# Kernel tuning notes

Measured on AMD Instinct MI355X. Metric: run time of the kernel, lower is better.

Reference implementation:

```python
import jax, jax.numpy as jnp
import numpy as np

A = 5            # atten_size
WIN = 2 * A + 1  # window size = 11


def _xavier(key, shape):
    fan_in, fan_out = shape[-2], shape[-1]
    std = np.sqrt(2.0 / (fan_in + fan_out))
    return (jax.random.normal(key, shape, jnp.float32) * std).astype(jnp.float32)


def setup_inputs() -> dict:
    key = jax.random.key(0)
    ks = jax.random.split(key, 8)
    B, S, D, H, O = 32768, 11, 128, 32, 2
    return {
        "x": jax.random.normal(ks[0], (B, S, D), jnp.float32),
        "W1": _xavier(ks[1], (D, H)),
        "b1": jnp.zeros((1, 1, H), jnp.float32),
        "Wq": _xavier(ks[2], (H, H)),
        "Wk": _xavier(ks[3], (H, H)),
        "Wv": _xavier(ks[4], (H, H)),
        "pos_enc": _xavier(ks[5], (1, WIN, H)),
        "Wo": _xavier(ks[6], (H, O)),
        "bo": jnp.zeros((1, 1, O), jnp.float32),
    }


def reference(x, W1, b1, Wq, Wk, Wv, pos_enc, Wo, bo):
    B, S, D = x.shape
    H = W1.shape[1]
    h = jax.nn.relu(x @ W1 + b1)                 # (B,S,H)
    h = h + pos_enc[:, :S, :]
    # sliding-window neighborhood, equivalent to torch pad+roll+stack:
    # x_nei[b,t,i] = h[b, t + (A - i)] with zero padding out of range
    padded = jnp.pad(h, ((0, 0), (A, A), (0, 0)))
    x_nei = jnp.stack([padded[:, 2 * A - i: 2 * A - i + S, :] for i in range(WIN)], axis=2)
    q = (h @ Wq)[:, :, None, :]                  # (B,S,1,H)
    keys = x_nei @ Wk
    vals = x_nei @ Wv
    scores = jnp.matmul(q, jnp.swapaxes(keys, -1, -2)) / jnp.sqrt(jnp.float32(H))
    # Faithful to torch.nn.Softmax(2): softmax over the singleton dim -> all ones
    attn_w = jax.nn.softmax(scores, axis=2)
    attn_out = jnp.matmul(attn_w, vals)[:, :, 0, :]  # (B,S,H)
    out = attn_out @ Wo + bo                     # (B,S,O)
    return out, attn_w
```

## Files before the change

kernel.cpp:

```cpp
#include <hip/hip_runtime.h>
#include <stdint.h>

#define NB   32768
#define SS   11
#define DD   128
#define HH   32
#define ROWS (NB * SS)
#define RPB  128
#define NBLK (ROWS / RPB)
#define TPB  256
#define XSTRD 68
#define TOT4 (ROWS * SS / 4)
#define AUXOFF (ROWS * 2)

__device__ __forceinline__ uint32_t f2bf_u(float f) {
    uint32_t u = __float_as_uint(f);
    return (u + 0x7fffu + ((u >> 16) & 1u)) >> 16;
}
__device__ __forceinline__ uint32_t pkbf(float lo, float hi) {
    return f2bf_u(lo) | (f2bf_u(hi) << 16);
}
__device__ __forceinline__ float dot2bf(uint32_t a, uint32_t b, float c) {
    float d;
    asm("v_dot2_f32_bf16 %0, %1, %2, %3" : "=v"(d) : "v"(a), "v"(b), "v"(c));
    return d;
}
__device__ __forceinline__ float xor32sum(float v) {
    float a = v, b = v;
    asm("v_permlane32_swap_b32 %0, %1" : "+v"(a), "+v"(b));
    return a + b;
}

__global__ __launch_bounds__(64) void setup_kernel(
    const float* __restrict__ Wv, const float* __restrict__ Wo,
    const float* __restrict__ pos, const float* __restrict__ bo,
    float* __restrict__ aux)
{
    __shared__ float M_s[HH * 2];
    __shared__ float pm_s[SS * 2];
    const int t = threadIdx.x;
    {
        int j = t >> 1, o = t & 1;
        float s = 0.f;
        #pragma unroll 8
        for (int k = 0; k < HH; ++k) s += Wv[j * HH + k] * Wo[k * 2 + o];
        M_s[t] = s;
        aux[t] = s;
    }
    __syncthreads();
    if (t < 2 * SS) {
        int u = t >> 1, o = t & 1;
        float s = 0.f;
        #pragma unroll 8
        for (int j = 0; j < HH; ++j) s += pos[u * HH + j] * M_s[j * 2 + o];
        pm_s[t] = s;
    }
    __syncthreads();
    if (t < 2 * SS) {
        int tt = t >> 1, o = t & 1;
        int lo = tt - 5 < 0 ? 0 : tt - 5;
        int hi = tt + 5 > SS - 1 ? SS - 1 : tt + 5;
        float s = bo[o];
        for (int u = lo; u <= hi; ++u) s += pm_s[u * 2 + o];
        aux[64 + t] = s;
    }
}

__global__ __launch_bounds__(TPB, 3) void g_kernel(
    const float* __restrict__ x, const float* __restrict__ W1,
    const float* __restrict__ b1, const float* __restrict__ aux,
    float* __restrict__ g)
{
    __shared__ uint32_t x_p[RPB * XSTRD];
    __shared__ uint32_t w_p[64 * HH];

    const int t   = threadIdx.x;
    const int blk = blockIdx.x;

    const float4* xsrc = (const float4*)(x + (size_t)blk * (RPB * DD));
    #pragma unroll
    for (int k = 0; k < 8; ++k) {
        int j = t + k * TPB;
        float4 v0 = xsrc[2 * j], v1 = xsrc[2 * j + 1];
        uint4 pv;
        pv.x = pkbf(v0.x, v0.y); pv.y = pkbf(v0.z, v0.w);
        pv.z = pkbf(v1.x, v1.y); pv.w = pkbf(v1.z, v1.w);
        int row = j >> 4, d8 = j & 15;
        *(uint4*)&x_p[row * XSTRD + d8 * 4] = pv;
    }
    #pragma unroll
    for (int k = 0; k < 8; ++k) {
        int i = t + k * TPB;
        int p = i >> 5, j = i & 31;
        w_p[i] = pkbf(W1[(2 * p) * HH + j], W1[(2 * p + 1) * HH + j]);
    }

    const int lane = t & 63, wave = t >> 6;
    const int cg = lane & 3;
    const int rg = (lane >> 2) & 7;
    const int kc = lane >> 5;
    const int j0 = cg * 8;
    const int rbase = wave * 32 + rg;

    float b1v[8], Mv[16];
    *(float4*)&b1v[0] = *(const float4*)&b1[j0];
    *(float4*)&b1v[4] = *(const float4*)&b1[j0 + 4];
    #pragma unroll
    for (int q = 0; q < 4; ++q)
        *(float4*)&Mv[q * 4] = *(const float4*)&aux[j0 * 2 + q * 4];
    __syncthreads();

    float acc[4][8] = {};
    #pragma unroll
    for (int i = 0; i < 8; ++i) {
        uint32_t xv[4][4], wv[4][8];
        #pragma unroll
        for (int rr = 0; rr < 4; ++rr)
            *(uint4*)xv[rr] = *(const uint4*)&x_p[(rbase + 8 * rr) * XSTRD + kc * 32 + i * 4];
        #pragma unroll
        for (int pp = 0; pp < 4; ++pp) {
            *(uint4*)&wv[pp][0] = *(const uint4*)&w_p[(kc * 32 + i * 4 + pp) * HH + j0];
            *(uint4*)&wv[pp][4] = *(const uint4*)&w_p[(kc * 32 + i * 4 + pp) * HH + j0 + 4];
        }
        #pragma unroll
        for (int rr = 0; rr < 4; ++rr)
            #pragma unroll
            for (int pp = 0; pp < 4; ++pp)
                #pragma unroll
                for (int c = 0; c < 8; ++c)
                    acc[rr][c] = dot2bf(xv[rr][pp], wv[pp][c], acc[rr][c]);
    }

    #pragma unroll
    for (int rr = 0; rr < 4; ++rr) {
        float s0 = 0.f, s1 = 0.f;
        #pragma unroll
        for (int c = 0; c < 8; ++c) {
            float full = xor32sum(acc[rr][c]);
            float y = fmaxf(full + b1v[c], 0.f);
            s0 = fmaf(y, Mv[c * 2], s0);
            s1 = fmaf(y, Mv[c * 2 + 1], s1);
        }
        s0 += __shfl_xor(s0, 1); s1 += __shfl_xor(s1, 1);
        s0 += __shfl_xor(s0, 2); s1 += __shfl_xor(s1, 2);
        if ((lane & 35) == 0) {
            int row = blk * RPB + rbase + 8 * rr;
            ((float2*)g)[row] = make_float2(s0, s1);
        }
    }
}

__global__ __launch_bounds__(256) void outones_kernel(
    const float* __restrict__ g, const float* __restrict__ aux,
    float* __restrict__ out1, float4* __restrict__ attn)
{
    int idx = blockIdx.x * 256 + threadIdx.x;
    attn[idx] = make_float4(1.f, 1.f, 1.f, 1.f);
    if (idx < ROWS) {
        int b = idx / SS, tt = idx - b * SS;
        const float2* gb = (const float2*)(g + (size_t)b * (2 * SS));
        int lo = tt - 5 < 0 ? 0 : tt - 5;
        int hi = tt + 5 > SS - 1 ? SS - 1 : tt + 5;
        float2 pw = *(const float2*)&aux[64 + tt * 2];
        float s0 = pw.x, s1 = pw.y;
        for (int u = lo; u <= hi; ++u) { float2 v = gb[u]; s0 += v.x; s1 += v.y; }
        ((float2*)out1)[idx] = make_float2(s0, s1);
    }
}

__global__ __launch_bounds__(256) void out_kernel(
    const float* __restrict__ g, const float* __restrict__ aux,
    float* __restrict__ out1)
{
    int idx = blockIdx.x * 256 + threadIdx.x;
    int b = idx / SS, tt = idx - b * SS;
    const float2* gb = (const float2*)(g + (size_t)b * (2 * SS));
    int lo = tt - 5 < 0 ? 0 : tt - 5;
    int hi = tt + 5 > SS - 1 ? SS - 1 : tt + 5;
    float2 pw = *(const float2*)&aux[64 + tt * 2];
    float s0 = pw.x, s1 = pw.y;
    for (int u = lo; u <= hi; ++u) { float2 v = gb[u]; s0 += v.x; s1 += v.y; }
    ((float2*)out1)[idx] = make_float2(s0, s1);
}
__global__ __launch_bounds__(256) void ones_kernel(float4* __restrict__ p)
{
    int i = blockIdx.x * 256 + threadIdx.x;
    p[i] = make_float4(1.f, 1.f, 1.f, 1.f);
}

extern "C" void kernel_launch(void* const* d_in, const int* in_sizes, int n_in,
                              void* d_out, int out_size, void* d_ws, size_t ws_size,
                              hipStream_t stream)
{
    const float* x   = (const float*)d_in[0];
    const float* W1  = (const float*)d_in[1];
    const float* b1  = (const float*)d_in[2];
    const float* Wv  = (const float*)d_in[5];
    const float* pos = (const float*)d_in[6];
    const float* Wo  = (const float*)d_in[7];
    const float* bo  = (const float*)d_in[8];

    float* out1 = (float*)d_out;
    float* attn = out1 + (size_t)ROWS * 2;

    const bool ws_ok = ws_size >= (size_t)(AUXOFF + 128) * sizeof(float);
    float* base = ws_ok ? (float*)d_ws : attn;
    float* g    = base;
    float* aux  = base + AUXOFF;

    setup_kernel<<<1, 64, 0, stream>>>(Wv, Wo, pos, bo, aux);
    g_kernel<<<NBLK, TPB, 0, stream>>>(x, W1, b1, aux, g);
    if (ws_ok) {
        outones_kernel<<<TOT4 / 256, 256, 0, stream>>>(g, aux, out1, (float4*)attn);
    } else {
        out_kernel<<<ROWS / 256, 256, 0, stream>>>(g, aux, out1);
        ones_kernel<<<TOT4 / 256, 256, 0, stream>>>((float4*)attn);
    }
}
```

Baseline: 54.97 us.

## Make g_kernel persistent with register-prefetch of next x tile

Converts the main GEMM kernel into a persistent grid of 768 blocks that loop over tiles. While computing the current tile from LDS, each block loads the next tile's x into 16 float4 registers, then converts and stores it to LDS after a barrier. This overlaps global memory latency with compute and amortizes the W1 packing, at the cost of higher register pressure (the kernel still requests 3 blocks per SM) and extra barriers.

```diff
diff --git a/kernel.cpp b/kernel.cpp
--- a/kernel.cpp
+++ b/kernel.cpp
@@ -1,16 +1,17 @@
 #include <hip/hip_runtime.h>
 #include <stdint.h>
 
-#define NB   32768
-#define SS   11
-#define DD   128
-#define HH   32
-#define ROWS (NB * SS)
-#define RPB  128
-#define NBLK (ROWS / RPB)
-#define TPB  256
+#define NB    32768
+#define SS    11
+#define DD    128
+#define HH    32
+#define ROWS  (NB * SS)
+#define RPB   128
+#define TILES (ROWS / RPB)
+#define GBLK  768
+#define TPB   256
 #define XSTRD 68
-#define TOT4 (ROWS * SS / 4)
+#define TOT4  (ROWS * SS / 4)
 #define AUXOFF (ROWS * 2)
 
 __device__ __forceinline__ uint32_t f2bf_u(float f) {
@@ -74,26 +75,8 @@
     __shared__ uint32_t x_p[RPB * XSTRD];
     __shared__ uint32_t w_p[64 * HH];
 
-    const int t   = threadIdx.x;
+    const int t = threadIdx.x;
     const int blk = blockIdx.x;
-
-    const float4* xsrc = (const float4*)(x + (size_t)blk * (RPB * DD));
-    #pragma unroll
-    for (int k = 0; k < 8; ++k) {
-        int j = t + k * TPB;
-        float4 v0 = xsrc[2 * j], v1 = xsrc[2 * j + 1];
-        uint4 pv;
-        pv.x = pkbf(v0.x, v0.y); pv.y = pkbf(v0.z, v0.w);
-        pv.z = pkbf(v1.x, v1.y); pv.w = pkbf(v1.z, v1.w);
-        int row = j >> 4, d8 = j & 15;
-        *(uint4*)&x_p[row * XSTRD + d8 * 4] = pv;
-    }
-    #pragma unroll
-    for (int k = 0; k < 8; ++k) {
-        int i = t + k * TPB;
-        int p = i >> 5, j = i & 31;
-        w_p[i] = pkbf(W1[(2 * p) * HH + j], W1[(2 * p + 1) * HH + j]);
-    }
 
     const int lane = t & 63, wave = t >> 6;
     const int cg = lane & 3;
@@ -108,45 +91,104 @@
     #pragma unroll
     for (int q = 0; q < 4; ++q)
         *(float4*)&Mv[q * 4] = *(const float4*)&aux[j0 * 2 + q * 4];
+
+    #pragma unroll
+    for (int k = 0; k < 8; ++k) {
+        int i = t + k * TPB;
+        int p = i >> 5, j = i & 31;
+        w_p[i] = pkbf(W1[(2 * p) * HH + j], W1[(2 * p + 1) * HH + j]);
+    }
+
+    int tile = blk;
+    float4 xr[16];
+    {
+        const float4* xs = (const float4*)(x + (size_t)tile * (RPB * DD));
+        #pragma unroll
+        for (int k = 0; k < 8; ++k) {
+            int j = t + k * TPB;
+            xr[2 * k]     = xs[2 * j];
+            xr[2 * k + 1] = xs[2 * j + 1];
+        }
+    }
+    #pragma unroll
+    for (int k = 0; k < 8; ++k) {
+        int j = t + k * TPB;
+        uint4 pv;
+        pv.x = pkbf(xr[2 * k].x, xr[2 * k].y);
+        pv.y = pkbf(xr[2 * k].z, xr[2 * k].w);
+        pv.z = pkbf(xr[2 * k + 1].x, xr[2 * k + 1].y);
+        pv.w = pkbf(xr[2 * k + 1].z, xr[2 * k + 1].w);
+        int row = j >> 4, d8 = j & 15;
+        *(uint4*)&x_p[row * XSTRD + d8 * 4] = pv;
+    }
     __syncthreads();
 
-    float acc[4][8] = {};
-    #pragma unroll
-    for (int i = 0; i < 8; ++i) {
-        uint32_t xv[4][4], wv[4][8];
-        #pragma unroll
-        for (int rr = 0; rr < 4; ++rr)
-            *(uint4*)xv[rr] = *(const uint4*)&x_p[(rbase + 8 * rr) * XSTRD + kc * 32 + i * 4];
-        #pragma unroll
-        for (int pp = 0; pp < 4; ++pp) {
-            *(uint4*)&wv[pp][0] = *(const uint4*)&w_p[(kc * 32 + i * 4 + pp) * HH + j0];
-            *(uint4*)&wv[pp][4] = *(const uint4*)&w_p[(kc * 32 + i * 4 + pp) * HH + j0 + 4];
-        }
-        #pragma unroll
-        for (int rr = 0; rr < 4; ++rr)
-            #pragma unroll
-            for (int pp = 0; pp < 4; ++pp)
+    for (;;) {
+        const int next = tile + GBLK;
+        if (next < TILES) {
+            const float4* xs = (const float4*)(x + (size_t)next * (RPB * DD));
+            #pragma unroll
+            for (int k = 0; k < 8; ++k) {
+                int j = t + k * TPB;
+                xr[2 * k]     = xs[2 * j];
+                xr[2 * k + 1] = xs[2 * j + 1];
+            }
+        }
+
+        float acc[4][8] = {};
+        #pragma unroll
+        for (int i = 0; i < 8; ++i) {
+            uint32_t xv[4][4];
+            #pragma unroll
+            for (int rr = 0; rr < 4; ++rr)
+                *(uint4*)xv[rr] =
+                    *(const uint4*)&x_p[(rbase + 8 * rr) * XSTRD + kc * 32 + i * 4];
+            #pragma unroll
+            for (int pp = 0; pp < 4; ++pp) {
+                uint32_t wv[8];
+                *(uint4*)&wv[0] = *(const uint4*)&w_p[(kc * 32 + i * 4 + pp) * HH + j0];
+                *(uint4*)&wv[4] = *(const uint4*)&w_p[(kc * 32 + i * 4 + pp) * HH + j0 + 4];
                 #pragma unroll
-                for (int c = 0; c < 8; ++c)
-                    acc[rr][c] = dot2bf(xv[rr][pp], wv[pp][c], acc[rr][c]);
-    }
-
-    #pragma unroll
-    for (int rr = 0; rr < 4; ++rr) {
-        float s0 = 0.f, s1 = 0.f;
-        #pragma unroll
-        for (int c = 0; c < 8; ++c) {
-            float full = xor32sum(acc[rr][c]);
-            float y = fmaxf(full + b1v[c], 0.f);
-            s0 = fmaf(y, Mv[c * 2], s0);
-            s1 = fmaf(y, Mv[c * 2 + 1], s1);
-        }
-        s0 += __shfl_xor(s0, 1); s1 += __shfl_xor(s1, 1);
-        s0 += __shfl_xor(s0, 2); s1 += __shfl_xor(s1, 2);
-        if ((lane & 35) == 0) {
-            int row = blk * RPB + rbase + 8 * rr;
-            ((float2*)g)[row] = make_float2(s0, s1);
-        }
+                for (int rr = 0; rr < 4; ++rr)
+                    #pragma unroll
+                    for (int c = 0; c < 8; ++c)
+                        acc[rr][c] = dot2bf(xv[rr][pp], wv[c], acc[rr][c]);
+            }
+        }
+
+        #pragma unroll
+        for (int rr = 0; rr < 4; ++rr) {
+            float s0 = 0.f, s1 = 0.f;
+            #pragma unroll
+            for (int c = 0; c < 8; ++c) {
+                float full = xor32sum(acc[rr][c]);
+                float y = fmaxf(full + b1v[c], 0.f);
+                s0 = fmaf(y, Mv[c * 2], s0);
+                s1 = fmaf(y, Mv[c * 2 + 1], s1);
+            }
+            s0 += __shfl_xor(s0, 1); s1 += __shfl_xor(s1, 1);
+            s0 += __shfl_xor(s0, 2); s1 += __shfl_xor(s1, 2);
+            if ((lane & 35) == 0) {
+                int row = tile * RPB + rbase + 8 * rr;
+                ((float2*)g)[row] = make_float2(s0, s1);
+            }
+        }
+
+        if (next >= TILES) break;
+        __syncthreads();
+        #pragma unroll
+        for (int k = 0; k < 8; ++k) {
+            int j = t + k * TPB;
+            uint4 pv;
+            pv.x = pkbf(xr[2 * k].x, xr[2 * k].y);
+            pv.y = pkbf(xr[2 * k].z, xr[2 * k].w);
+            pv.z = pkbf(xr[2 * k + 1].x, xr[2 * k + 1].y);
+            pv.w = pkbf(xr[2 * k + 1].z, xr[2 * k + 1].w);
+            int row = j >> 4, d8 = j & 15;
+            *(uint4*)&x_p[row * XSTRD + d8 * 4] = pv;
+        }
+        __syncthreads();
+        tile = next;
     }
 }
 
@@ -209,7 +251,7 @@
     float* aux  = base + AUXOFF;
 
     setup_kernel<<<1, 64, 0, stream>>>(Wv, Wo, pos, bo, aux);
-    g_kernel<<<NBLK, TPB, 0, stream>>>(x, W1, b1, aux, g);
+    g_kernel<<<GBLK, TPB, 0, stream>>>(x, W1, b1, aux, g);
     if (ws_ok) {
         outones_kernel<<<TOT4 / 256, 256, 0, stream>>>(g, aux, out1, (float4*)attn);
     } else {
```

Measured after the change: 104.0 us. 89.2% more time.

## Double block size, use hardware bf16 pack, split setup reduction, reorder dot loop

Applied to the files above, without the earlier changes.

The main kernel now processes 256 rows per block with 512 threads, so each block stages more x rows while the W1 tile is loaded once per block. Bf16 packing uses the v_cvt_pk_bf16_f32 instruction instead of manual round-to-nearest bit arithmetic. The dot-product loop loads W1 values per pp step to lower register pressure. The setup kernel splits each reduction across 4 lanes with shuffles. The larger blocks and two-block occupancy bound change LDS use and scheduling, which could reduce latency hiding.

```diff
diff --git a/kernel.cpp b/kernel.cpp
--- a/kernel.cpp
+++ b/kernel.cpp
@@ -1,24 +1,22 @@
 #include <hip/hip_runtime.h>
 #include <stdint.h>
 
-#define NB   32768
-#define SS   11
-#define DD   128
-#define HH   32
-#define ROWS (NB * SS)
-#define RPB  128
-#define NBLK (ROWS / RPB)
-#define TPB  256
+#define NB    32768
+#define SS    11
+#define DD    128
+#define HH    32
+#define ROWS  (NB * SS)
+#define RPB   256
+#define NBLK  (ROWS / RPB)
+#define TPB   512
 #define XSTRD 68
-#define TOT4 (ROWS * SS / 4)
+#define TOT4  (ROWS * SS / 4)
 #define AUXOFF (ROWS * 2)
 
-__device__ __forceinline__ uint32_t f2bf_u(float f) {
-    uint32_t u = __float_as_uint(f);
-    return (u + 0x7fffu + ((u >> 16) & 1u)) >> 16;
-}
 __device__ __forceinline__ uint32_t pkbf(float lo, float hi) {
-    return f2bf_u(lo) | (f2bf_u(hi) << 16);
+    uint32_t r;
+    asm("v_cvt_pk_bf16_f32 %0, %1, %2" : "=v"(r) : "v"(lo), "v"(hi));
+    return r;
 }
 __device__ __forceinline__ float dot2bf(uint32_t a, uint32_t b, float c) {
     float d;
@@ -31,7 +29,7 @@
     return a + b;
 }
 
-__global__ __launch_bounds__(64) void setup_kernel(
+__global__ __launch_bounds__(256) void setup_kernel(
     const float* __restrict__ Wv, const float* __restrict__ Wo,
     const float* __restrict__ pos, const float* __restrict__ bo,
     float* __restrict__ aux)
@@ -40,12 +38,15 @@
     __shared__ float pm_s[SS * 2];
     const int t = threadIdx.x;
     {
-        int j = t >> 1, o = t & 1;
+        int i2 = t >> 2, kq = t & 3;
+        int j = i2 >> 1, o = i2 & 1;
         float s = 0.f;
-        #pragma unroll 8
-        for (int k = 0; k < HH; ++k) s += Wv[j * HH + k] * Wo[k * 2 + o];
-        M_s[t] = s;
-        aux[t] = s;
+        #pragma unroll
+        for (int k = kq * 8; k < kq * 8 + 8; ++k)
+            s += Wv[j * HH + k] * Wo[k * 2 + o];
+        s += __shfl_xor(s, 1);
+        s += __shfl_xor(s, 2);
+        if (kq == 0) { M_s[i2] = s; aux[i2] = s; }
     }
     __syncthreads();
     if (t < 2 * SS) {
@@ -66,7 +67,7 @@
     }
 }
 
-__global__ __launch_bounds__(TPB, 3) void g_kernel(
+__global__ __launch_bounds__(TPB, 2) void g_kernel(
     const float* __restrict__ x, const float* __restrict__ W1,
     const float* __restrict__ b1, const float* __restrict__ aux,
     float* __restrict__ g)
@@ -89,7 +90,7 @@
         *(uint4*)&x_p[row * XSTRD + d8 * 4] = pv;
     }
     #pragma unroll
-    for (int k = 0; k < 8; ++k) {
+    for (int k = 0; k < 4; ++k) {
         int i = t + k * TPB;
         int p = i >> 5, j = i & 31;
         w_p[i] = pkbf(W1[(2 * p) * HH + j], W1[(2 * p + 1) * HH + j]);
@@ -113,22 +114,22 @@
     float acc[4][8] = {};
     #pragma unroll
     for (int i = 0; i < 8; ++i) {
-        uint32_t xv[4][4], wv[4][8];
+        uint32_t xv[4][4];
         #pragma unroll
         for (int rr = 0; rr < 4; ++rr)
-            *(uint4*)xv[rr] = *(const uint4*)&x_p[(rbase + 8 * rr) * XSTRD + kc * 32 + i * 4];
+            *(uint4*)xv[rr] =
+                *(const uint4*)&x_p[(rbase + 8 * rr) * XSTRD + kc * 32 + i * 4];
         #pragma unroll
         for (int pp = 0; pp < 4; ++pp) {
-            *(uint4*)&wv[pp][0] = *(const uint4*)&w_p[(kc * 32 + i * 4 + pp) * HH + j0];
-            *(uint4*)&wv[pp][4] = *(const uint4*)&w_p[(kc * 32 + i * 4 + pp) * HH + j0 + 4];
-        }
-        #pragma unroll
-        for (int rr = 0; rr < 4; ++rr)
+            uint32_t wv[8];
+            *(uint4*)&wv[0] = *(const uint4*)&w_p[(kc * 32 + i * 4 + pp) * HH + j0];
+            *(uint4*)&wv[4] = *(const uint4*)&w_p[(kc * 32 + i * 4 + pp) * HH + j0 + 4];
             #pragma unroll
-            for (int pp = 0; pp < 4; ++pp)
+            for (int rr = 0; rr < 4; ++rr)
                 #pragma unroll
                 for (int c = 0; c < 8; ++c)
-                    acc[rr][c] = dot2bf(xv[rr][pp], wv[pp][c], acc[rr][c]);
+                    acc[rr][c] = dot2bf(xv[rr][pp], wv[c], acc[rr][c]);
+        }
     }
 
     #pragma unroll
@@ -208,7 +209,7 @@
     float* g    = base;
     float* aux  = base + AUXOFF;
 
-    setup_kernel<<<1, 64, 0, stream>>>(Wv, Wo, pos, bo, aux);
+    setup_kernel<<<1, 256, 0, stream>>>(Wv, Wo, pos, bo, aux);
     g_kernel<<<NBLK, TPB, 0, stream>>>(x, W1, b1, aux, g);
     if (ws_ok) {
         outones_kernel<<<TOT4 / 256, 256, 0, stream>>>(g, aux, out1, (float4*)attn);
```

Measured after the change: 55.51 us. No clear change (+1.0%).
